# Kernel tuning notes

Measured on AMD Instinct MI355X. Metric: run time of the kernel, lower is better.

## Reference

```python
import jax, jax.numpy as jnp
import numpy as np

FS = 4096.0
TRAIN_KERNEL = 4
TRAIN_STRIDE = 0.25
BATCH = 1024
NPERSEG = 4096          # fftlength * fs
NOVERLAP = NPERSEG // 2 # default overlap
FL, FH = 20.0, 500.0


def _welch(data):
    """Faithful port of _torch_welch with average='mean' (which is a SUM over segments
    in the original code), off by the same constant factor as the original."""
    N, nsample = data.shape
    nstride = NPERSEG - NOVERLAP
    nseg = int(np.ceil((nsample - NPERSEG) / nstride)) + 1
    # frame indices [nseg, nperseg] (static numpy -> cheap gather)
    idx = np.arange(nseg)[:, None] * nstride + np.arange(NPERSEG)[None, :]
    frames = data[:, idx]                                   # [N, nseg, nperseg]
    n = np.arange(NPERSEG)
    window = (0.5 - 0.5 * np.cos(2.0 * np.pi * n / NPERSEG)).astype(np.float32) * 2.0  # periodic hann * 2
    fd = jnp.fft.rfft(frames * window, axis=-1)             # [N, nseg, nfreq]
    power = jnp.real(fd) ** 2 + jnp.imag(fd) ** 2
    psd = jnp.sum(power, axis=1)                            # original 'mean' branch uses sum
    T = nsample * FS
    return psd / T                                          # [N, nfreq]


def setup_inputs() -> dict:
    key = jax.random.key(0)
    k1, k2 = jax.random.split(key)
    T = int(TRAIN_KERNEL * FS)  # 16384
    pred = jax.random.normal(k1, (BATCH, T), dtype=jnp.float32)
    target = jax.random.normal(k2, (BATCH, T), dtype=jnp.float32)
    return {"pred": pred, "target": target}


def reference(pred, target):
    res = target - pred
    s = int(TRAIN_STRIDE * FS)                     # 1024 samples per stride
    shape_x = int(TRAIN_KERNEL / TRAIN_STRIDE)     # 16
    # cross[i] = res[:, i*s:(i+1)*s].flatten() -> reshape/transpose, no loop
    def to_cross(x):
        return x[:, : shape_x * s].reshape(BATCH, shape_x, s).transpose(1, 0, 2).reshape(shape_x, BATCH * s)
    cross_res = to_cross(res)
    cross_target = to_cross(target)

    psd_res = _welch(cross_res)                    # [shape_x, nfreq]
    psd_target = _welch(cross_target)

    nfreq = NPERSEG // 2 + 1
    freq = np.linspace(0.0, FS / 2.0, nfreq)
    mask = jnp.asarray((FL < freq) & (freq < FH))
    dfreq = float(freq[1] - freq[0])
    scale = FH - FL

    psd_res = jnp.where(mask, psd_res, 0.0)
    psd_ratio = psd_res / psd_target
    loss = jnp.sum(psd_ratio, axis=1) * dfreq / scale  # [shape_x]
    return jnp.mean(loss[-8:]) * loss.shape[0]
```

## Files before the change

kernel.cpp:

```cpp
#include <hip/hip_runtime.h>

#define NSEG 511
#define NROWS 8
#define ROW0 8
#define K0 21
#define KEND 500
#define NFREQ 479
#define ACC_STRIDE 512

__device__ __forceinline__ int dr_pos(int k) {
    int p = k & 3;
    p = (p << 2) | ((k >> 2) & 3);
    p = (p << 2) | ((k >> 4) & 3);
    p = (p << 2) | ((k >> 6) & 3);
    p = (p << 2) | ((k >> 8) & 3);
    p = (p << 1) | ((k >> 10) & 1);
    return p;
}

__device__ __forceinline__ float2 cmul(float2 a, float2 b) {
    return make_float2(a.x * b.x - a.y * b.y, a.x * b.y + a.y * b.x);
}

__global__ __launch_bounds__(256)
void psd_kernel(const float* __restrict__ pred,
                const float* __restrict__ target,
                float* __restrict__ acc) {
    __shared__ float2 buf[2048];

    const int bid = blockIdx.x;
    const int seg = bid % NSEG;
    const int row = (bid / NSEG) % NROWS + ROW0;
    const int sig = bid / (NSEG * NROWS);
    const int tid = threadIdx.x;

    const float4* tgt4 = (const float4*)target;
    const float4* prd4 = (const float4*)pred;
    float4* b4 = (float4*)buf;
    const float wstep = 6.28318530717958647692f / 4096.0f;
    #pragma unroll
    for (int it = 0; it < 4; ++it) {
        int t4 = tid + 256 * it;
        int b  = 2 * seg + (t4 >> 8);
        int g  = b * 4096 + (row << 8) + (t4 & 255);
        float4 v = tgt4[g];
        if (sig == 0) {
            float4 p = prd4[g];
            v.x -= p.x; v.y -= p.y; v.z -= p.z; v.w -= p.w;
        }
        float t0 = (float)(4 * t4);
        float w0 = 1.0f - __cosf(wstep * t0);
        float w1 = 1.0f - __cosf(wstep * (t0 + 1.0f));
        float w2 = 1.0f - __cosf(wstep * (t0 + 2.0f));
        float w3 = 1.0f - __cosf(wstep * (t0 + 3.0f));
        b4[t4] = make_float4(v.x * w0, v.y * w1, v.z * w2, v.w * w3);
    }
    __syncthreads();

    #pragma unroll
    for (int st = 0; st < 5; ++st) {
        const int lnb = 9 - 2 * st;
        const int nb  = 1 << lnb;
        const int q   = nb;
        const float theta = -6.28318530717958647692f / (float)(nb << 2);
        #pragma unroll
        for (int u = 0; u < 2; ++u) {
            int t = tid + 256 * u;
            int j = t & (nb - 1);
            int base = ((t >> lnb) << (lnb + 2)) + j;
            float2 x0 = buf[base];
            float2 x1 = buf[base + q];
            float2 x2 = buf[base + 2 * q];
            float2 x3 = buf[base + 3 * q];
            float2 s0 = make_float2(x0.x + x2.x, x0.y + x2.y);
            float2 d0 = make_float2(x0.x - x2.x, x0.y - x2.y);
            float2 s1 = make_float2(x1.x + x3.x, x1.y + x3.y);
            float2 d1 = make_float2(x1.x - x3.x, x1.y - x3.y);
            float2 c0 = make_float2(s0.x + s1.x, s0.y + s1.y);
            float2 c2 = make_float2(s0.x - s1.x, s0.y - s1.y);
            float2 c1 = make_float2(d0.x + d1.y, d0.y - d1.x);
            float2 c3 = make_float2(d0.x - d1.y, d0.y + d1.x);
            float sn, cs;
            __sincosf(theta * (float)j, &sn, &cs);
            float2 w1 = make_float2(cs, sn);
            float2 w2 = make_float2(cs * cs - sn * sn, 2.0f * cs * sn);
            float2 w3 = cmul(w2, w1);
            buf[base]         = c0;
            buf[base + q]     = cmul(c1, w1);
            buf[base + 2 * q] = cmul(c2, w2);
            buf[base + 3 * q] = cmul(c3, w3);
        }
        __syncthreads();
    }

    #pragma unroll
    for (int u = 0; u < 4; ++u) {
        int t = tid + 256 * u;
        float4 v = b4[t];
        b4[t] = make_float4(v.x + v.z, v.y + v.w, v.x - v.z, v.y - v.w);
    }
    __syncthreads();

    #pragma unroll
    for (int rr = 0; rr < 2; ++rr) {
        int k = K0 + tid + 256 * rr;
        if (k < KEND) {
            float2 zk = buf[dr_pos(k)];
            float2 zn = buf[dr_pos(2048 - k)];
            float Ex = 0.5f * (zk.x + zn.x);
            float Ey = 0.5f * (zk.y - zn.y);
            float Ox = 0.5f * (zk.y + zn.y);
            float Oy = -0.5f * (zk.x - zn.x);
            float sn, cs;
            __sincosf(-6.28318530717958647692f * (float)k / 4096.0f, &sn, &cs);
            float xr = Ex + Ox * cs - Oy * sn;
            float xi = Ey + Ox * sn + Oy * cs;
            float pw = xr * xr + xi * xi;
            atomicAdd(&acc[(sig * NROWS + (row - ROW0)) * ACC_STRIDE + (k - K0)], pw);
        }
    }
}

__global__ __launch_bounds__(256)
void reduce_kernel(const float* __restrict__ acc, float* __restrict__ out) {
    __shared__ float sh[256];
    int tid = threadIdx.x;
    float sum = 0.0f;
    for (int n = tid; n < NROWS * NFREQ; n += 256) {
        int r = n / NFREQ;
        int k = n % NFREQ;
        sum += acc[r * ACC_STRIDE + k] / acc[(NROWS + r) * ACC_STRIDE + k];
    }
    sh[tid] = sum;
    __syncthreads();
    for (int s = 128; s > 0; s >>= 1) {
        if (tid < s) sh[tid] += sh[tid + s];
        __syncthreads();
    }
    if (tid == 0) out[0] = sh[0] * (1.0f / 240.0f);
}

extern "C" void kernel_launch(void* const* d_in, const int* in_sizes, int n_in,
                              void* d_out, int out_size, void* d_ws, size_t ws_size,
                              hipStream_t stream) {
    const float* pred = (const float*)d_in[0];
    const float* target = (const float*)d_in[1];
    float* acc = (float*)d_ws;

    hipMemsetAsync(acc, 0, 2 * NROWS * ACC_STRIDE * sizeof(float), stream);
    psd_kernel<<<2 * NROWS * NSEG, 256, 0, stream>>>(pred, target, acc);
    reduce_kernel<<<1, 256, 0, stream>>>(acc, (float*)d_out);
}
```

Before: 199.8 us.

## Switch to radix-8 register FFT with swizzled LDS and fuse final reduction

Replaces the five radix-4 shared-memory FFT stages with three radix-8 stages done in registers plus a final radix-4 pass. The window is computed with one sincos per pair, and LDS indices use an XOR swizzle to reduce bank conflicts. This cuts barriers and shared-memory traffic. The separate reduce kernel is removed: a last-block-done counter lets the final block compute the loss, saving one launch at the cost of an atomic and a fence per block.

```diff
diff --git a/kernel.cpp b/kernel.cpp
--- a/kernel.cpp
+++ b/kernel.cpp
@@ -7,26 +7,63 @@
 #define KEND 500
 #define NFREQ 479
 #define ACC_STRIDE 512
+#define NBLOCKS (2 * NROWS * NSEG)
+
+__device__ __forceinline__ int sw(int i) { return i ^ (((i >> 5) & 7) << 2); }
 
 __device__ __forceinline__ int dr_pos(int k) {
-    int p = k & 3;
-    p = (p << 2) | ((k >> 2) & 3);
-    p = (p << 2) | ((k >> 4) & 3);
-    p = (p << 2) | ((k >> 6) & 3);
-    p = (p << 2) | ((k >> 8) & 3);
-    p = (p << 1) | ((k >> 10) & 1);
-    return p;
+    return ((k >> 9) & 3) + 4 * ((k >> 6) & 7) + 32 * ((k >> 3) & 7) + 256 * (k & 7);
 }
 
 __device__ __forceinline__ float2 cmul(float2 a, float2 b) {
-    return make_float2(a.x * b.x - a.y * b.y, a.x * b.y + a.y * b.x);
+    return make_float2(fmaf(a.x, b.x, -a.y * b.y), fmaf(a.x, b.y, a.y * b.x));
+}
+__device__ __forceinline__ float2 cadd(float2 a, float2 b) { return make_float2(a.x + b.x, a.y + b.y); }
+__device__ __forceinline__ float2 csub(float2 a, float2 b) { return make_float2(a.x - b.x, a.y - b.y); }
+
+__device__ __forceinline__ void dft8(float2* x) {
+    const float C45 = 0.70710678118654752440f;
+    float2 t0 = cadd(x[0], x[4]), u0 = csub(x[0], x[4]);
+    float2 t1 = cadd(x[1], x[5]), u1 = csub(x[1], x[5]);
+    float2 t2 = cadd(x[2], x[6]), u2 = csub(x[2], x[6]);
+    float2 t3 = cadd(x[3], x[7]), u3 = csub(x[3], x[7]);
+    float2 s0 = cadd(t0, t2), d0 = csub(t0, t2);
+    float2 s1 = cadd(t1, t3), d1 = csub(t1, t3);
+    float2 v1 = make_float2(C45 * (u1.x + u1.y), C45 * (u1.y - u1.x));
+    float2 v2 = make_float2(u2.y, -u2.x);
+    float2 v3 = make_float2(C45 * (u3.y - u3.x), -C45 * (u3.x + u3.y));
+    float2 s2 = cadd(u0, v2), d2 = csub(u0, v2);
+    float2 s3 = cadd(v1, v3), d3 = csub(v1, v3);
+    float2 mid1 = make_float2(d1.y, -d1.x);
+    float2 mid3 = make_float2(d3.y, -d3.x);
+    x[0] = cadd(s0, s1); x[4] = csub(s0, s1);
+    x[2] = cadd(d0, mid1); x[6] = csub(d0, mid1);
+    x[1] = cadd(s2, s3); x[5] = csub(s2, s3);
+    x[3] = cadd(d2, mid3); x[7] = csub(d2, mid3);
+}
+
+__device__ __forceinline__ void twiddle8(float2* x, float ang) {
+    float s, c;
+    __sincosf(ang, &s, &c);
+    float2 w1 = make_float2(c, s);
+    float2 w2 = cmul(w1, w1);
+    float2 w3 = cmul(w2, w1);
+    float2 w4 = cmul(w2, w2);
+    float2 w5 = cmul(w4, w1);
+    float2 w6 = cmul(w3, w3);
+    float2 w7 = cmul(w4, w3);
+    x[1] = cmul(x[1], w1); x[2] = cmul(x[2], w2); x[3] = cmul(x[3], w3);
+    x[4] = cmul(x[4], w4); x[5] = cmul(x[5], w5); x[6] = cmul(x[6], w6);
+    x[7] = cmul(x[7], w7);
 }
 
 __global__ __launch_bounds__(256)
 void psd_kernel(const float* __restrict__ pred,
                 const float* __restrict__ target,
-                float* __restrict__ acc) {
+                float* __restrict__ acc, int* __restrict__ counter,
+                float* __restrict__ out) {
     __shared__ float2 buf[2048];
+    __shared__ int is_last;
 
     const int bid = blockIdx.x;
     const int seg = bid % NSEG;
@@ -34,70 +71,68 @@
     const int sig = bid / (NSEG * NROWS);
     const int tid = threadIdx.x;
 
-    const float4* tgt4 = (const float4*)target;
-    const float4* prd4 = (const float4*)pred;
-    float4* b4 = (float4*)buf;
-    const float wstep = 6.28318530717958647692f / 4096.0f;
+    const float2* t2p = (const float2*)target;
+    const float2* p2p = (const float2*)pred;
+
+    float2 x[8];
+
+    const float WA = 3.06796157577128245e-3f;
+    const float CD = 0.99999882344642529f;
+    const float SD = 1.53398018628476550e-3f;
     #pragma unroll
-    for (int it = 0; it < 4; ++it) {
-        int t4 = tid + 256 * it;
-        int b  = 2 * seg + (t4 >> 8);
-        int g  = b * 4096 + (row << 8) + (t4 & 255);
-        float4 v = tgt4[g];
-        if (sig == 0) {
-            float4 p = prd4[g];
-            v.x -= p.x; v.y -= p.y; v.z -= p.z; v.w -= p.w;
-        }
-        float t0 = (float)(4 * t4);
-        float w0 = 1.0f - __cosf(wstep * t0);
-        float w1 = 1.0f - __cosf(wstep * (t0 + 1.0f));
-        float w2 = 1.0f - __cosf(wstep * (t0 + 2.0f));
-        float w3 = 1.0f - __cosf(wstep * (t0 + 3.0f));
-        b4[t4] = make_float4(v.x * w0, v.y * w1, v.z * w2, v.w * w3);
+    for (int r = 0; r < 8; ++r) {
+        int idx2 = (2 * seg + (r >> 1)) * 8192 + row * 512 + tid + 256 * (r & 1);
+        float2 v = t2p[idx2];
+        if (sig == 0) { float2 p = p2p[idx2]; v.x -= p.x; v.y -= p.y; }
+        int m = tid + 256 * r;
+        float sa, ca;
+        __sincosf((float)m * WA, &sa, &ca);
+        float w0 = 1.0f - ca;
+        float w1 = 1.0f - (ca * CD - sa * SD);
+        x[r] = make_float2(v.x * w0, v.y * w1);
     }
+
+    dft8(x);
+    twiddle8(x, (float)tid * -3.06796157577128245e-3f);
+    #pragma unroll
+    for (int p = 0; p < 8; ++p) buf[sw(tid + 256 * p)] = x[p];
     __syncthreads();
 
+    const int pb = tid >> 5, q0 = tid & 31;
+    const int baseB = q0 + 256 * pb;
     #pragma unroll
-    for (int st = 0; st < 5; ++st) {
-        const int lnb = 9 - 2 * st;
-        const int nb  = 1 << lnb;
-        const int q   = nb;
-        const float theta = -6.28318530717958647692f / (float)(nb << 2);
-        #pragma unroll
-        for (int u = 0; u < 2; ++u) {
-            int t = tid + 256 * u;
-            int j = t & (nb - 1);
-            int base = ((t >> lnb) << (lnb + 2)) + j;
-            float2 x0 = buf[base];
-            float2 x1 = buf[base + q];
-            float2 x2 = buf[base + 2 * q];
-            float2 x3 = buf[base + 3 * q];
-            float2 s0 = make_float2(x0.x + x2.x, x0.y + x2.y);
-            float2 d0 = make_float2(x0.x - x2.x, x0.y - x2.y);
-            float2 s1 = make_float2(x1.x + x3.x, x1.y + x3.y);
-            float2 d1 = make_float2(x1.x - x3.x, x1.y - x3.y);
-            float2 c0 = make_float2(s0.x + s1.x, s0.y + s1.y);
-            float2 c2 = make_float2(s0.x - s1.x, s0.y - s1.y);
-            float2 c1 = make_float2(d0.x + d1.y, d0.y - d1.x);
-            float2 c3 = make_float2(d0.x - d1.y, d0.y + d1.x);
-            float sn, cs;
-            __sincosf(theta * (float)j, &sn, &cs);
-            float2 w1 = make_float2(cs, sn);
-            float2 w2 = make_float2(cs * cs - sn * sn, 2.0f * cs * sn);
-            float2 w3 = cmul(w2, w1);
-            buf[base]         = c0;
-            buf[base + q]     = cmul(c1, w1);
-            buf[base + 2 * q] = cmul(c2, w2);
-            buf[base + 3 * q] = cmul(c3, w3);
-        }
-        __syncthreads();
-    }
+    for (int j = 0; j < 8; ++j) x[j] = buf[sw(baseB + 32 * j)];
+    dft8(x);
+    twiddle8(x, (float)q0 * -2.45436926061702596e-2f);
+    #pragma unroll
+    for (int j = 0; j < 8; ++j) buf[sw(baseB + 32 * j)] = x[j];
+    __syncthreads();
 
+    const int pb2 = tid >> 5, j2 = (tid >> 2) & 7, mq = tid & 3;
+    const int baseC = mq + 32 * j2 + 256 * pb2;
     #pragma unroll
-    for (int u = 0; u < 4; ++u) {
-        int t = tid + 256 * u;
-        float4 v = b4[t];
-        b4[t] = make_float4(v.x + v.z, v.y + v.w, v.x - v.z, v.y - v.w);
+    for (int i = 0; i < 8; ++i) x[i] = buf[sw(baseC + 4 * i)];
+    dft8(x);
+    twiddle8(x, (float)mq * -1.96349540849362077e-1f);
+    #pragma unroll
+    for (int i = 0; i < 8; ++i) buf[sw(baseC + 4 * i)] = x[i];
+    __syncthreads();
+
+    float4* b4 = (float4*)buf;
+    #pragma unroll
+    for (int g = 0; g < 2; ++g) {
+        int pbase = sw(4 * (tid + 256 * g));
+        float4 lo = b4[(pbase >> 1)];
+        float4 hi = b4[(pbase >> 1) + 1];
+        float2 a0 = make_float2(lo.x, lo.y), a1 = make_float2(lo.z, lo.w);
+        float2 a2 = make_float2(hi.x, hi.y), a3 = make_float2(hi.z, hi.w);
+        float2 S0 = cadd(a0, a2), D0 = csub(a0, a2);
+        float2 S1 = cadd(a1, a3), D1 = csub(a1, a3);
+        float2 mi = make_float2(D1.y, -D1.x);
+        float2 X0 = cadd(S0, S1), X2 = csub(S0, S1);
+        float2 X1 = cadd(D0, mi), X3 = csub(D0, mi);
+        b4[(pbase >> 1)]     = make_float4(X0.x, X0.y, X1.x, X1.y);
+        b4[(pbase >> 1) + 1] = make_float4(X2.x, X2.y, X3.x, X3.y);
     }
     __syncthreads();
 
@@ -105,39 +140,47 @@
     for (int rr = 0; rr < 2; ++rr) {
         int k = K0 + tid + 256 * rr;
         if (k < KEND) {
-            float2 zk = buf[dr_pos(k)];
-            float2 zn = buf[dr_pos(2048 - k)];
+            float2 zk = buf[sw(dr_pos(k))];
+            float2 zn = buf[sw(dr_pos(2048 - k))];
             float Ex = 0.5f * (zk.x + zn.x);
             float Ey = 0.5f * (zk.y - zn.y);
             float Ox = 0.5f * (zk.y + zn.y);
             float Oy = -0.5f * (zk.x - zn.x);
             float sn, cs;
-            __sincosf(-6.28318530717958647692f * (float)k / 4096.0f, &sn, &cs);
+            __sincosf(-1.53398078788564123e-3f * (float)k, &sn, &cs);
             float xr = Ex + Ox * cs - Oy * sn;
             float xi = Ey + Ox * sn + Oy * cs;
             float pw = xr * xr + xi * xi;
             atomicAdd(&acc[(sig * NROWS + (row - ROW0)) * ACC_STRIDE + (k - K0)], pw);
         }
     }
-}
 
-__global__ __launch_bounds__(256)
-void reduce_kernel(const float* __restrict__ acc, float* __restrict__ out) {
-    __shared__ float sh[256];
-    int tid = threadIdx.x;
-    float sum = 0.0f;
-    for (int n = tid; n < NROWS * NFREQ; n += 256) {
-        int r = n / NFREQ;
-        int k = n % NFREQ;
-        sum += acc[r * ACC_STRIDE + k] / acc[(NROWS + r) * ACC_STRIDE + k];
+    __syncthreads();
+    if (tid == 0) {
+        __threadfence();
+        int old = atomicAdd(counter, 1);
+        is_last = (old == NBLOCKS - 1) ? 1 : 0;
     }
-    sh[tid] = sum;
     __syncthreads();
-    for (int s = 128; s > 0; s >>= 1) {
-        if (tid < s) sh[tid] += sh[tid + s];
+    if (is_last) {
+        float sum = 0.0f;
+        for (int n = tid; n < NROWS * NFREQ; n += 256) {
+            int r = n / NFREQ, k = n % NFREQ;
+            float num = __hip_atomic_load(&acc[r * ACC_STRIDE + k],
+                                          __ATOMIC_RELAXED, __HIP_MEMORY_SCOPE_AGENT);
+            float den = __hip_atomic_load(&acc[(NROWS + r) * ACC_STRIDE + k],
+                                          __ATOMIC_RELAXED, __HIP_MEMORY_SCOPE_AGENT);
+            sum += num / den;
+        }
+        float* shf = (float*)buf;
+        shf[tid] = sum;
         __syncthreads();
+        for (int s2 = 128; s2 > 0; s2 >>= 1) {
+            if (tid < s2) shf[tid] += shf[tid + s2];
+            __syncthreads();
+        }
+        if (tid == 0) out[0] = shf[0] * (1.0f / 240.0f);
     }
-    if (tid == 0) out[0] = sh[0] * (1.0f / 240.0f);
 }
 
 extern "C" void kernel_launch(void* const* d_in, const int* in_sizes, int n_in,
@@ -146,8 +189,8 @@
     const float* pred = (const float*)d_in[0];
     const float* target = (const float*)d_in[1];
     float* acc = (float*)d_ws;
+    int* counter = (int*)(acc + 2 * NROWS * ACC_STRIDE);
 
-    hipMemsetAsync(acc, 0, 2 * NROWS * ACC_STRIDE * sizeof(float), stream);
-    psd_kernel<<<2 * NROWS * NSEG, 256, 0, stream>>>(pred, target, acc);
-    reduce_kernel<<<1, 256, 0, stream>>>(acc, (float*)d_out);
+    hipMemsetAsync(d_ws, 0, (2 * NROWS * ACC_STRIDE + 1) * sizeof(float), stream);
+    psd_kernel<<<NBLOCKS, 256, 0, stream>>>(pred, target, acc, counter, (float*)d_out);
 }
```

Result: slower. 348.0 us (+74.2%).
